# Kernel tuning notes

Hardware: AMD Instinct MI355X
Metric: run time of the kernel (lower is better)

## Reference

```python
import jax, jax.numpy as jnp
import numpy as np

GRID_DIMS = (64, 64, 64)
GRID_LOWER = np.array([0.0, 0.0, 0.0], np.float32)
GRID_STEPS = np.array([0.015625, 0.015625, 0.015625], np.float32)
RADIUS = 0.03125
STENCIL = 2  # ceil(radius / step)


def _poly6(d2, h):
    # standard SPH poly6 smoothing kernel: 315/(64 pi h^9) (h^2 - d^2)^3, d <= h
    c = np.float32(315.0 / (64.0 * np.pi * h ** 9))
    return jnp.where(d2 <= h * h, c * (h * h - d2) ** 3, 0.0)


def particles2grid(locs, data, density):
    # locs [B,N,3], data [B,N,C], density [B,N] -> grid [B,X,Y,Z,C]
    B, N, _ = locs.shape
    C = data.shape[-1]
    X, Y, Z = GRID_DIMS
    dims = jnp.array(GRID_DIMS, jnp.int32)
    r = jnp.arange(-STENCIL, STENCIL + 1)
    offs = jnp.stack(jnp.meshgrid(r, r, r, indexing='ij'), -1).reshape(-1, 3)  # [K,3]
    base = jnp.floor((locs - GRID_LOWER) / GRID_STEPS).astype(jnp.int32)        # [B,N,3]
    cells = base[:, :, None, :] + offs                                          # [B,N,K,3]
    centers = GRID_LOWER + (cells.astype(locs.dtype) + 0.5) * GRID_STEPS
    d2 = jnp.sum((centers - locs[:, :, None, :]) ** 2, -1)                      # [B,N,K]
    w = _poly6(d2, RADIUS)
    w = jnp.where(jnp.all((cells >= 0) & (cells < dims), -1), w, 0.0)
    contrib = w[..., None] * (data / density[..., None])[:, :, None, :]         # [B,N,K,C]
    cells = jnp.clip(cells, 0, dims - 1)
    flat = (cells[..., 0] * Y + cells[..., 1]) * Z + cells[..., 2]              # [B,N,K]

    def splat(f, c):
        return jnp.zeros((X * Y * Z, C), data.dtype).at[f.reshape(-1)].add(c.reshape(-1, C))

    return jax.vmap(splat)(flat, contrib).reshape(B, X, Y, Z, C)


def grid2particles(grid, locs):
    # trilinear interpolation of grid [B,X,Y,Z,C] at particle locations [B,N,3]
    B, X, Y, Z, C = grid.shape
    dims = jnp.array([X, Y, Z], jnp.int32)
    pos = (locs - GRID_LOWER) / GRID_STEPS - 0.5                                # cell-center coords
    i0 = jnp.floor(pos).astype(jnp.int32)
    frac = pos - i0.astype(locs.dtype)
    gflat = grid.reshape(B, X * Y * Z, C)
    gather = jax.vmap(lambda g, f: g[f])                                        # [B,N] -> [B,N,C]
    out = jnp.zeros((B, locs.shape[1], C), grid.dtype)
    for dx in (0, 1):
        for dy in (0, 1):
            for dz in (0, 1):
                off = jnp.array([dx, dy, dz], jnp.int32)
                idx = i0 + off
                wd = jnp.where(off == 1, frac, 1.0 - frac)                      # [B,N,3]
                w = wd[..., 0] * wd[..., 1] * wd[..., 2]
                w = jnp.where(jnp.all((idx >= 0) & (idx < dims), -1), w, 0.0)
                idx = jnp.clip(idx, 0, dims - 1)
                flat = (idx[..., 0] * Y + idx[..., 1]) * Z + idx[..., 2]
                out = out + w[..., None] * gather(gflat, flat)
    return out


def conv3d(x, w, b):
    y = jax.lax.conv_general_dilated(x, w, (1, 1, 1), 'SAME',
                                     dimension_numbers=('NCDHW', 'OIDHW', 'NCDHW'))
    return y + b[None, :, None, None, None]


def prelu(x, a):
    return jnp.where(x >= 0, x, a * x)


def setup_inputs() -> dict:
    key = jax.random.key(0)
    ks = jax.random.split(key, 8)
    B, N = 2, 32768
    Cin, K, Cout = 4, 32, 4
    s = lambda fan: np.float32(1.0 / np.sqrt(fan * 27))
    return {
        'locs': jax.random.uniform(ks[0], (B, N, 3), jnp.float32),
        'data': jax.random.normal(ks[1], (B, N, Cin), jnp.float32),
        'density': jax.random.uniform(ks[2], (B, N), jnp.float32, 0.5, 1.5),
        'W0': jax.random.normal(ks[3], (K, Cin, 3, 3, 3), jnp.float32) * s(Cin),
        'b0': jnp.zeros((K,), jnp.float32),
        'W1': jax.random.normal(ks[4], (K, K, 3, 3, 3), jnp.float32) * s(K),
        'b1': jnp.zeros((K,), jnp.float32),
        'W2': jax.random.normal(ks[5], (K, K, 3, 3, 3), jnp.float32) * s(K),
        'b2': jnp.zeros((K,), jnp.float32),
        'W3': jax.random.normal(ks[6], (Cout, K, 3, 3, 3), jnp.float32) * s(K),
        'b3': jnp.zeros((Cout,), jnp.float32),
        'a0': jnp.full((1,), 0.25, jnp.float32),
        'a1': jnp.full((1,), 0.25, jnp.float32),
        'a2': jnp.full((1,), 0.25, jnp.float32),
    }


def reference(locs, data, density, W0, b0, W1, b1, W2, b2, W3, b3, a0, a1, a2):
    grid = particles2grid(locs, data, density)            # [B,X,Y,Z,Cin]
    g = jnp.transpose(grid, (0, 4, 1, 2, 3))              # NCDHW
    g = prelu(conv3d(g, W0, b0), a0)
    g = prelu(conv3d(g, W1, b1), a1)
    g = prelu(conv3d(g, W2, b2), a2)
    g = conv3d(g, W3, b3)
    g = jnp.transpose(g, (0, 2, 3, 4, 1))                 # [B,X,Y,Z,Cout]
    return grid2particles(g, locs)                        # [B,N,Cout]
```

## Files before the change

### kernel.cpp

```cpp
#include <hip/hip_runtime.h>

#define BATCH 2
#define NPART 32768
#define GD 64
#define NVOX (BATCH * GD * GD * GD)

typedef unsigned short ushortT;
typedef __attribute__((ext_vector_type(8))) short short8;
typedef __attribute__((ext_vector_type(16))) float float16;

__device__ __forceinline__ float poly6_c() {
    const double H9 = 1.0 / 35184372088832.0;
    return (float)(315.0 / (64.0 * 3.14159265358979323846 * H9));
}

__device__ __forceinline__ ushortT bf16_rne(float f) {
    unsigned int u = __float_as_uint(f);
    u = (u + 0x7fffu + ((u >> 16) & 1u)) >> 16;
    return (ushortT)u;
}

__device__ __forceinline__ int imax(int a, int b) { return a > b ? a : b; }
__device__ __forceinline__ int imin(int a, int b) { return a < b ? a : b; }

__global__ void zero_ints_kernel(int* __restrict__ p, int n) {
    int t = blockIdx.x * blockDim.x + threadIdx.x;
    if (t < n) p[t] = 0;
}

__global__ __launch_bounds__(256) void bin_count_kernel(
    const float* __restrict__ locs, int* __restrict__ counts) {
    int t = blockIdx.x * blockDim.x + threadIdx.x;
    if (t >= BATCH * NPART) return;
    int b = t >> 15;
    int bx = ((int)floorf(locs[t * 3 + 0] * 64.0f)) >> 1;
    int by = ((int)floorf(locs[t * 3 + 1] * 64.0f)) >> 1;
    int bz = ((int)floorf(locs[t * 3 + 2] * 64.0f)) >> 1;
    atomicAdd(&counts[b * 32768 + ((bx * 32) + by) * 32 + bz], 1);
}

__global__ __launch_bounds__(256) void scanA_kernel(
    const int* __restrict__ counts, int* __restrict__ offsets,
    int* __restrict__ blockSum) {
    __shared__ int sh[256];
    int tid = threadIdx.x, g = blockIdx.x;
    int v = counts[g * 256 + tid];
    sh[tid] = v;
    __syncthreads();
    for (int off = 1; off < 256; off <<= 1) {
        int u = (tid >= off) ? sh[tid - off] : 0;
        __syncthreads();
        sh[tid] += u;
        __syncthreads();
    }
    offsets[g * 256 + tid] = sh[tid] - v;
    if (tid == 255) blockSum[g] = sh[255];
}

__global__ __launch_bounds__(256) void scanB_kernel(
    int* __restrict__ offsets, const int* __restrict__ blockSum) {
    __shared__ int sh[256];
    int tid = threadIdx.x, g = blockIdx.x;
    sh[tid] = (tid < g) ? blockSum[tid] : 0;
    __syncthreads();
    for (int off = 128; off > 0; off >>= 1) {
        if (tid < off) sh[tid] += sh[tid + off];
        __syncthreads();
    }
    offsets[g * 256 + tid] += sh[0];
    if (g == 255 && tid == 255) offsets[65536] = BATCH * NPART;
}

__global__ __launch_bounds__(256) void bin_scatter_kernel(
    const float* __restrict__ locs, const float* __restrict__ data,
    const float* __restrict__ density, const int* __restrict__ offsets,
    int* __restrict__ cursor, float* __restrict__ payload) {
    int t = blockIdx.x * blockDim.x + threadIdx.x;
    if (t >= BATCH * NPART) return;
    int b = t >> 15;
    float px = locs[t * 3 + 0];
    float py = locs[t * 3 + 1];
    float pz = locs[t * 3 + 2];
    int bx = ((int)floorf(px * 64.0f)) >> 1;
    int by = ((int)floorf(py * 64.0f)) >> 1;
    int bz = ((int)floorf(pz * 64.0f)) >> 1;
    int bb = b * 32768 + ((bx * 32) + by) * 32 + bz;
    int slot = atomicAdd(&cursor[bb], 1);
    int idx = offsets[bb] + slot;
    float inv_d = 1.0f / density[t];
    float4 p0 = {px, py, pz, data[t * 4 + 0] * inv_d};
    float4 p1 = {data[t * 4 + 1] * inv_d, data[t * 4 + 2] * inv_d,
                 data[t * 4 + 3] * inv_d, 0.f};
    *(float4*)(payload + idx * 8)     = p0;
    *(float4*)(payload + idx * 8 + 4) = p1;
}

__global__ __launch_bounds__(256) void splat_gather_kernel(
    const float* __restrict__ payload, const int* __restrict__ offsets,
    ushortT* __restrict__ g8) {
    __shared__ float plist[256 * 8];
    __shared__ int segS[36];
    __shared__ int segP[37];
    __shared__ int shTot[1];

    int wg = blockIdx.x;
    int sb = wg & 511, b = wg >> 9;
    int X0 = (sb >> 6) * 8, Y0 = ((sb >> 3) & 7) * 8, Z0 = (sb & 7) * 8;
    int tid = threadIdx.x;

    int bxlo = imax(0, (X0 - 2) >> 1), bxhi = imin(31, (X0 + 9) >> 1);
    int bylo = imax(0, (Y0 - 2) >> 1), byhi = imin(31, (Y0 + 9) >> 1);
    int bzlo = imax(0, (Z0 - 2) >> 1), bzhi = imin(31, (Z0 + 9) >> 1);
    int ny = byhi - bylo + 1;
    int ns = (bxhi - bxlo + 1) * ny;
    if (tid < ns) {
        int bx = bxlo + tid / ny, by = bylo + tid % ny;
        int row = b * 32768 + (bx * 32 + by) * 32;
        int s = offsets[row + bzlo];
        int e = offsets[row + bzhi + 1];
        segS[tid] = s;
        segP[tid] = e - s;
    }
    __syncthreads();
    if (tid == 0) {
        int p = 0;
        for (int k = 0; k < ns; ++k) { int len = segP[k]; segP[k] = p; p += len; }
        segP[ns] = p;
        shTot[0] = p;
    }
    __syncthreads();

    const float step = 0.015625f;
    const float h2 = 0.03125f * 0.03125f;
    const float cc = poly6_c();
    int total = shTot[0];

    int l = tid & 63, w = tid >> 6;
    int cx = X0 + 4 * (w >> 1) + (l >> 4);
    int cy = Y0 + 4 * (w & 1) + ((l >> 2) & 3);
    int cz0 = Z0 + (l & 3);
    float xc  = ((float)cx  + 0.5f) * step;
    float yc  = ((float)cy  + 0.5f) * step;
    float zc0 = ((float)cz0 + 0.5f) * step;
    float zc1 = zc0 + 4.0f * step;

    float a00 = 0.f, a01 = 0.f, a02 = 0.f, a03 = 0.f;
    float a10 = 0.f, a11 = 0.f, a12 = 0.f, a13 = 0.f;

    int nchunks = (total + 255) >> 8;
    for (int ch = 0; ch < nchunks; ++ch) {
        __syncthreads();
        int jj = (ch << 8) + tid;
        if (jj < total) {
            int k = 0;
            while (jj >= segP[k + 1]) ++k;
            int idx = segS[k] + (jj - segP[k]);
            *(float4*)(plist + tid * 8)     = *(const float4*)(payload + idx * 8);
            *(float4*)(plist + tid * 8 + 4) = *(const float4*)(payload + idx * 8 + 4);
        }
        __syncthreads();
        int cnt = imin(256, total - (ch << 8));
        for (int p = 0; p < cnt; ++p) {
            float4 pa = *(const float4*)(plist + p * 8);
            float dx = pa.x - xc, dy = pa.y - yc;
            float dxy2 = fmaf(dy, dy, dx * dx);
            if (!__any(dxy2 <= h2)) continue;
            float4 pv = *(const float4*)(plist + p * 8 + 4);
            float dz0 = pa.z - zc0;
            float d20 = fmaf(dz0, dz0, dxy2);
            float u0 = fmaxf(h2 - d20, 0.f);
            float w0 = (cc * u0) * (u0 * u0);
            a00 = fmaf(w0, pa.w, a00);
            a01 = fmaf(w0, pv.x, a01);
            a02 = fmaf(w0, pv.y, a02);
            a03 = fmaf(w0, pv.z, a03);
            float dz1 = pa.z - zc1;
            float d21 = fmaf(dz1, dz1, dxy2);
            float u1 = fmaxf(h2 - d21, 0.f);
            float w1 = (cc * u1) * (u1 * u1);
            a10 = fmaf(w1, pa.w, a10);
            a11 = fmaf(w1, pv.x, a11);
            a12 = fmaf(w1, pv.y, a12);
            a13 = fmaf(w1, pv.z, a13);
        }
    }

    size_t cellBase = (size_t)(((b * 64 + cx) * 64 + cy) * 64);
    short8 o;
    o[0] = (short)bf16_rne(a00); o[1] = (short)bf16_rne(a01);
    o[2] = (short)bf16_rne(a02); o[3] = (short)bf16_rne(a03);
    o[4] = 0; o[5] = 0; o[6] = 0; o[7] = 0;
    *(short8*)(g8 + (cellBase + cz0) * 8) = o;
    o[0] = (short)bf16_rne(a10); o[1] = (short)bf16_rne(a11);
    o[2] = (short)bf16_rne(a12); o[3] = (short)bf16_rne(a13);
    *(short8*)(g8 + (cellBase + cz0 + 4) * 8) = o;
}

__global__ void repack_all_kernel(
    const float* __restrict__ W0, const float* __restrict__ W1,
    const float* __restrict__ W2, const float* __restrict__ W3,
    short* __restrict__ Bp) {
    int t = blockIdx.x * blockDim.x + threadIdx.x;
    if (t >= 176 * 512) return;
    int kt = t >> 9;
    const float* W; int O, I, CINP, ktL;
    if (kt < 14)       { W = W0; O = 32; I = 4;  CINP = 8;  ktL = kt; }
    else if (kt < 68)  { W = W1; O = 32; I = 32; CINP = 32; ktL = kt - 14; }
    else if (kt < 122) { W = W2; O = 32; I = 32; CINP = 32; ktL = kt - 68; }
    else               { W = W3; O = 4;  I = 32; CINP = 32; ktL = kt - 122; }
    int l = (t >> 3) & 63, j = t & 7;
    int n = l & 31, q = l >> 5;
    int k = ktL * 16 + 8 * q + j;
    int tap = k / CINP;
    int ic  = k - tap * CINP;
    float v = 0.f;
    if (tap < 27 && ic < I && n < O) v = W[(n * I + ic) * 27 + tap];
    Bp[t] = (short)bf16_rne(v);
}

template <int ICG, int KT, bool FINAL>
__global__ __launch_bounds__(256) void mfma_conv_kernel(
    const ushortT* __restrict__ in, const short* __restrict__ Bpack,
    const float* __restrict__ bias, const float* __restrict__ alpha,
    void* __restrict__ outv) {
    constexpr int CIN = ICG * 8;
    __shared__ short lds[12 * ICG * 66 * 8];
    int wg = ((blockIdx.x & 7) << 9) | (blockIdx.x >> 3);
    int yp = wg & 31, x = (wg >> 5) & 63, b = wg >> 11;
    int y0 = yp * 2;
    int tid = threadIdx.x;

    const int NCH = 12 * ICG * 66;
    for (int cc = tid; cc < NCH; cc += 256) {
        int col = cc / (ICG * 66);
        int rem = cc - col * (ICG * 66);
        int icg = rem / 66;
        int z66 = rem - icg * 66;
        int gx = x + (col >> 2) - 1;
        int gy = y0 + (col & 3) - 1;
        int z  = z66 - 1;
        short8 v = short8{0,0,0,0,0,0,0,0};
        if ((unsigned)gx < 64u && (unsigned)gy < 64u && (unsigned)z < 64u)
            v = *(const short8*)(in + ((size_t)(((b * 64 + gx) * 64 + gy) * 64 + z)) * CIN + icg * 8);
        *(short8*)(lds + cc * 8) = v;
    }
    __syncthreads();

    int l = tid & 63, w = tid >> 6;
    int ycol = w >> 1, mz = (w & 1) * 32;
    int n = l & 31, q = l >> 5;

    float bval = FINAL ? (n < 4 ? bias[n] : 0.f) : bias[n];
    float16 acc;
#pragma unroll
    for (int r = 0; r < 16; ++r) acc[r] = bval;

    const short* bp = Bpack + (size_t)l * 8;
    int laneBase = (mz + (l & 31)) * 8;
    int ycolOfs  = ycol * (ICG * 66) * 8;

#pragma unroll
    for (int kt = 0; kt < KT; ++kt) {
        short8 bfrag = *(const short8*)(bp + kt * 512);
        int aofs;
        if constexpr (ICG == 1) {
            int tap0 = kt * 2, tap1 = kt * 2 + 1;
            if (tap1 > 26) tap1 = 26;
            int dx0 = tap0 / 9, r0 = tap0 - dx0 * 9, dy0 = r0 / 3, dz0 = r0 - dy0 * 3;
            int dx1 = tap1 / 9, r1 = tap1 - dx1 * 9, dy1 = r1 / 3, dz1 = r1 - dy1 * 3;
            int c0 = ((dx0 * 4 + dy0) * 66 + dz0) * 8;
            int c1 = ((dx1 * 4 + dy1) * 66 + dz1) * 8;
            aofs = q ? c1 : c0;
        } else {
            int tap = kt >> 1;
            int dx = tap / 9, rr = tap - dx * 9, dy = rr / 3, dz = rr - dy * 3;
            int icg = (kt & 1) * 2 + q;
            aofs = (((dx * 4 + dy) * ICG + icg) * 66 + dz) * 8;
        }
        short8 afrag = *(const short8*)(lds + aofs + ycolOfs + laneBase);
        acc = __builtin_amdgcn_mfma_f32_32x32x16_bf16(afrag, bfrag, acc, 0, 0, 0);
    }

    int ygl = y0 + ycol;
    size_t base = (size_t)(((b * 64 + x) * 64 + ygl) * 64);
    if (FINAL) {
        float* out = (float*)outv;
        if (n < 4) {
#pragma unroll
            for (int r = 0; r < 16; ++r) {
                int z = mz + (r & 3) + 8 * (r >> 2) + 4 * q;
                out[(base + z) * 4 + n] = acc[r];
            }
        }
    } else {
        float a = alpha[0];
        ushortT* out = (ushortT*)outv;
#pragma unroll
        for (int r = 0; r < 16; ++r) {
            int z = mz + (r & 3) + 8 * (r >> 2) + 4 * q;
            float v = acc[r];
            v = v >= 0.f ? v : a * v;
            out[(base + z) * 32 + n] = bf16_rne(v);
        }
    }
}

__global__ __launch_bounds__(256) void gather_kernel(
    const float* __restrict__ grid, const float* __restrict__ locs,
    float* __restrict__ out) {
    int t = blockIdx.x * blockDim.x + threadIdx.x;
    if (t >= BATCH * NPART) return;
    int b = t >> 15;

    float px = locs[t * 3 + 0] * 64.0f - 0.5f;
    float py = locs[t * 3 + 1] * 64.0f - 0.5f;
    float pz = locs[t * 3 + 2] * 64.0f - 0.5f;
    int ix = (int)floorf(px);
    int iy = (int)floorf(py);
    int iz = (int)floorf(pz);
    float fx = px - (float)ix;
    float fy = py - (float)iy;
    float fz = pz - (float)iz;

    const float* gb = grid + (size_t)b * GD * GD * GD * 4;
    float o0 = 0.f, o1 = 0.f, o2 = 0.f, o3 = 0.f;

#pragma unroll
    for (int dx = 0; dx < 2; ++dx) {
        int x = ix + dx;
        if ((unsigned)x > 63u) continue;
        float wx = dx ? fx : 1.0f - fx;
#pragma unroll
        for (int dy = 0; dy < 2; ++dy) {
            int y = iy + dy;
            if ((unsigned)y > 63u) continue;
            float wy = dy ? fy : 1.0f - fy;
#pragma unroll
            for (int dz = 0; dz < 2; ++dz) {
                int z = iz + dz;
                if ((unsigned)z > 63u) continue;
                float wz = dz ? fz : 1.0f - fz;
                float w = wx * wy * wz;
                const float4 g = *(const float4*)(gb + (size_t)(((x * GD) + y) * GD + z) * 4);
                o0 += w * g.x; o1 += w * g.y; o2 += w * g.z; o3 += w * g.w;
            }
        }
    }
    out[t * 4 + 0] = o0;
    out[t * 4 + 1] = o1;
    out[t * 4 + 2] = o2;
    out[t * 4 + 3] = o3;
}

extern "C" void kernel_launch(void* const* d_in, const int* in_sizes, int n_in,
                              void* d_out, int out_size, void* d_ws, size_t ws_size,
                              hipStream_t stream) {
    const float* locs    = (const float*)d_in[0];
    const float* data    = (const float*)d_in[1];
    const float* density = (const float*)d_in[2];
    const float* W0 = (const float*)d_in[3];
    const float* b0 = (const float*)d_in[4];
    const float* W1 = (const float*)d_in[5];
    const float* b1 = (const float*)d_in[6];
    const float* W2 = (const float*)d_in[7];
    const float* b2 = (const float*)d_in[8];
    const float* W3 = (const float*)d_in[9];
    const float* b3 = (const float*)d_in[10];
    const float* a0 = (const float*)d_in[11];
    const float* a1 = (const float*)d_in[12];
    const float* a2 = (const float*)d_in[13];
    float* out = (float*)d_out;

    char* ws = (char*)d_ws;
    ushortT* g8  = (ushortT*)(ws);
    ushortT* gA  = (ushortT*)(ws + 8388608);
    ushortT* gB  = (ushortT*)(ws + 41943040);
    float*  gF   = (float*)(ws + 75497472);
    short*  Bp   = (short*)(ws + 83886080);
    short*  Bp0  = Bp;
    short*  Bp1  = Bp + 14 * 512;
    short*  Bp2  = Bp + 68 * 512;
    short*  Bp3  = Bp + 122 * 512;
    int*   counts   = (int*)(ws + 84066304);
    int*   cursor   = (int*)(ws + 84328448);
    int*   offsets  = (int*)(ws + 84590592);
    int*   blockSum = (int*)(ws + 84852752);
    float* payload  = (float*)(ws + 84853888);

    zero_ints_kernel<<<(131072 + 255) / 256, 256, 0, stream>>>(counts, 131072);
    bin_count_kernel<<<(BATCH * NPART) / 256, 256, 0, stream>>>(locs, counts);
    scanA_kernel<<<256, 256, 0, stream>>>(counts, offsets, blockSum);
    scanB_kernel<<<256, 256, 0, stream>>>(offsets, blockSum);
    bin_scatter_kernel<<<(BATCH * NPART) / 256, 256, 0, stream>>>(
        locs, data, density, offsets, cursor, payload);

    repack_all_kernel<<<(176 * 512 + 255) / 256, 256, 0, stream>>>(W0, W1, W2, W3, Bp);

    splat_gather_kernel<<<BATCH * 512, 256, 0, stream>>>(payload, offsets, g8);

    const int CGRID = BATCH * 64 * 32;
    mfma_conv_kernel< 1, 14, false><<<CGRID, 256, 0, stream>>>(g8, Bp0, b0, a0, gA);
    mfma_conv_kernel< 4, 54, false><<<CGRID, 256, 0, stream>>>(gA, Bp1, b1, a1, gB);
    mfma_conv_kernel< 4, 54, false><<<CGRID, 256, 0, stream>>>(gB, Bp2, b2, a2, gA);
    mfma_conv_kernel< 4, 54, true ><<<CGRID, 256, 0, stream>>>(gA, Bp3, b3, b3, gF);

    gather_kernel<<<(BATCH * NPART) / 256, 256, 0, stream>>>(gF, locs, out);
}
```

Baseline: 298.9 us.

## Retile conv blocks to 2x2x32 output and stage halos via direct global-to-LDS loads

Each conv workgroup changes from a 1x2x64 output column to a 2x2x32 tile, with the four waves spread over x and y. The LDS halo drops from 12x66 to 16x34 voxels per channel group, so fewer redundant halo bytes are loaded per output. The staging loop now uses global_load_lds with 16-byte transfers, and out-of-bounds voxels read from a zeroed guard buffer instead of using a register round trip. This needs a zguard region that the widened zero kernel clears, and the different tile shape changes the LDS access and bank patterns.

Result: faster. 267.1 us (-10.6%).

```diff
diff --git a/kernel.cpp b/kernel.cpp
--- a/kernel.cpp
+++ b/kernel.cpp
@@ -22,6 +22,12 @@
 
 __device__ __forceinline__ int imax(int a, int b) { return a > b ? a : b; }
 __device__ __forceinline__ int imin(int a, int b) { return a < b ? a : b; }
+
+__device__ __forceinline__ void load_lds16(const void* g, void* l) {
+    __builtin_amdgcn_global_load_lds(
+        (const __attribute__((address_space(1))) void*)g,
+        (__attribute__((address_space(3))) void*)l, 16, 0, 0);
+}
 
 __global__ void zero_ints_kernel(int* __restrict__ p, int n) {
     int t = blockIdx.x * blockDim.x + threadIdx.x;
@@ -222,32 +228,37 @@
 __global__ __launch_bounds__(256) void mfma_conv_kernel(
     const ushortT* __restrict__ in, const short* __restrict__ Bpack,
     const float* __restrict__ bias, const float* __restrict__ alpha,
-    void* __restrict__ outv) {
+    const float* __restrict__ zguard, void* __restrict__ outv) {
     constexpr int CIN = ICG * 8;
-    __shared__ short lds[12 * ICG * 66 * 8];
+    constexpr int NCH = 16 * ICG * 34;
+    __shared__ short lds[NCH * 8];
     int wg = ((blockIdx.x & 7) << 9) | (blockIdx.x >> 3);
-    int yp = wg & 31, x = (wg >> 5) & 63, b = wg >> 11;
-    int y0 = yp * 2;
+    int zh = wg & 1, yp = (wg >> 1) & 31, xp = (wg >> 6) & 31, b = wg >> 11;
+    int X0 = xp * 2, Y0 = yp * 2, Z0 = zh * 32;
     int tid = threadIdx.x;
 
-    const int NCH = 12 * ICG * 66;
-    for (int cc = tid; cc < NCH; cc += 256) {
-        int col = cc / (ICG * 66);
-        int rem = cc - col * (ICG * 66);
-        int icg = rem / 66;
-        int z66 = rem - icg * 66;
-        int gx = x + (col >> 2) - 1;
-        int gy = y0 + (col & 3) - 1;
-        int z  = z66 - 1;
-        short8 v = short8{0,0,0,0,0,0,0,0};
-        if ((unsigned)gx < 64u && (unsigned)gy < 64u && (unsigned)z < 64u)
-            v = *(const short8*)(in + ((size_t)(((b * 64 + gx) * 64 + gy) * 64 + z)) * CIN + icg * 8);
-        *(short8*)(lds + cc * 8) = v;
+    const ushortT* inb = in + (size_t)b * (64 * 64 * 64 * CIN);
+#pragma unroll
+    for (int it = 0; it < (NCH + 255) / 256; ++it) {
+        int ccid = it * 256 + tid;
+        if (ccid < NCH) {
+            int col = ccid / (ICG * 34);
+            int rem = ccid - col * (ICG * 34);
+            int icg = rem / 34;
+            int zi  = rem - icg * 34;
+            int gx = X0 + (col >> 2) - 1;
+            int gy = Y0 + (col & 3) - 1;
+            int gz = Z0 + zi - 1;
+            const void* src = (const void*)zguard;
+            if ((unsigned)gx < 64u && (unsigned)gy < 64u && (unsigned)gz < 64u)
+                src = (const void*)(inb + ((size_t)(((gx * 64) + gy) * 64 + gz)) * CIN + icg * 8);
+            load_lds16(src, (void*)(lds + ccid * 8));
+        }
     }
     __syncthreads();
 
     int l = tid & 63, w = tid >> 6;
-    int ycol = w >> 1, mz = (w & 1) * 32;
+    int wx = w >> 1, wy = w & 1;
     int n = l & 31, q = l >> 5;
 
     float bval = FINAL ? (n < 4 ? bias[n] : 0.f) : bias[n];
@@ -256,8 +267,7 @@
     for (int r = 0; r < 16; ++r) acc[r] = bval;
 
     const short* bp = Bpack + (size_t)l * 8;
-    int laneBase = (mz + (l & 31)) * 8;
-    int ycolOfs  = ycol * (ICG * 66) * 8;
+    int laneZ = (l & 31) * 8;
 
 #pragma unroll
     for (int kt = 0; kt < KT; ++kt) {
@@ -268,27 +278,26 @@
             if (tap1 > 26) tap1 = 26;
             int dx0 = tap0 / 9, r0 = tap0 - dx0 * 9, dy0 = r0 / 3, dz0 = r0 - dy0 * 3;
             int dx1 = tap1 / 9, r1 = tap1 - dx1 * 9, dy1 = r1 / 3, dz1 = r1 - dy1 * 3;
-            int c0 = ((dx0 * 4 + dy0) * 66 + dz0) * 8;
-            int c1 = ((dx1 * 4 + dy1) * 66 + dz1) * 8;
+            int c0 = (((wx + dx0) * 4 + (wy + dy0)) * 34 + dz0) * 8;
+            int c1 = (((wx + dx1) * 4 + (wy + dy1)) * 34 + dz1) * 8;
             aofs = q ? c1 : c0;
         } else {
             int tap = kt >> 1;
             int dx = tap / 9, rr = tap - dx * 9, dy = rr / 3, dz = rr - dy * 3;
             int icg = (kt & 1) * 2 + q;
-            aofs = (((dx * 4 + dy) * ICG + icg) * 66 + dz) * 8;
-        }
-        short8 afrag = *(const short8*)(lds + aofs + ycolOfs + laneBase);
+            aofs = ((((wx + dx) * 4 + (wy + dy)) * ICG + icg) * 34 + dz) * 8;
+        }
+        short8 afrag = *(const short8*)(lds + aofs + laneZ);
         acc = __builtin_amdgcn_mfma_f32_32x32x16_bf16(afrag, bfrag, acc, 0, 0, 0);
     }
 
-    int ygl = y0 + ycol;
-    size_t base = (size_t)(((b * 64 + x) * 64 + ygl) * 64);
+    size_t base = (size_t)(((b * 64 + X0 + wx) * 64 + (Y0 + wy)) * 64) + Z0;
     if (FINAL) {
         float* out = (float*)outv;
         if (n < 4) {
 #pragma unroll
             for (int r = 0; r < 16; ++r) {
-                int z = mz + (r & 3) + 8 * (r >> 2) + 4 * q;
+                int z = (r & 3) + 8 * (r >> 2) + 4 * q;
                 out[(base + z) * 4 + n] = acc[r];
             }
         }
@@ -297,7 +306,7 @@
         ushortT* out = (ushortT*)outv;
 #pragma unroll
         for (int r = 0; r < 16; ++r) {
-            int z = mz + (r & 3) + 8 * (r >> 2) + 4 * q;
+            int z = (r & 3) + 8 * (r >> 2) + 4 * q;
             float v = acc[r];
             v = v >= 0.f ? v : a * v;
             out[(base + z) * 32 + n] = bf16_rne(v);
@@ -381,13 +390,14 @@
     short*  Bp1  = Bp + 14 * 512;
     short*  Bp2  = Bp + 68 * 512;
     short*  Bp3  = Bp + 122 * 512;
+    float* zguard   = (float*)(ws + 84066240);
     int*   counts   = (int*)(ws + 84066304);
     int*   cursor   = (int*)(ws + 84328448);
     int*   offsets  = (int*)(ws + 84590592);
     int*   blockSum = (int*)(ws + 84852752);
     float* payload  = (float*)(ws + 84853888);
 
-    zero_ints_kernel<<<(131072 + 255) / 256, 256, 0, stream>>>(counts, 131072);
+    zero_ints_kernel<<<(131088 + 255) / 256, 256, 0, stream>>>((int*)zguard, 131088);
     bin_count_kernel<<<(BATCH * NPART) / 256, 256, 0, stream>>>(locs, counts);
     scanA_kernel<<<256, 256, 0, stream>>>(counts, offsets, blockSum);
     scanB_kernel<<<256, 256, 0, stream>>>(offsets, blockSum);
@@ -398,11 +408,11 @@
 
     splat_gather_kernel<<<BATCH * 512, 256, 0, stream>>>(payload, offsets, g8);
 
-    const int CGRID = BATCH * 64 * 32;
-    mfma_conv_kernel< 1, 14, false><<<CGRID, 256, 0, stream>>>(g8, Bp0, b0, a0, gA);
-    mfma_conv_kernel< 4, 54, false><<<CGRID, 256, 0, stream>>>(gA, Bp1, b1, a1, gB);
-    mfma_conv_kernel< 4, 54, false><<<CGRID, 256, 0, stream>>>(gB, Bp2, b2, a2, gA);
-    mfma_conv_kernel< 4, 54, true ><<<CGRID, 256, 0, stream>>>(gA, Bp3, b3, b3, gF);
+    const int CGRID = 4096;
+    mfma_conv_kernel< 1, 14, false><<<CGRID, 256, 0, stream>>>(g8, Bp0, b0, a0, zguard, gA);
+    mfma_conv_kernel< 4, 54, false><<<CGRID, 256, 0, stream>>>(gA, Bp1, b1, a1, zguard, gB);
+    mfma_conv_kernel< 4, 54, false><<<CGRID, 256, 0, stream>>>(gB, Bp2, b2, a2, zguard, gA);
+    mfma_conv_kernel< 4, 54, true ><<<CGRID, 256, 0, stream>>>(gA, Bp3, b3, b3, zguard, gF);
 
     gather_kernel<<<(BATCH * NPART) / 256, 256, 0, stream>>>(gF, locs, out);
 }
```
